# Optimization experiments

Measured on AMD Instinct MI355X. Metric: run time of the kernel, lower is better.

Reference implementation:

```python
import jax, jax.numpy as jnp
import numpy as np

DIM = 32          # image/vq dim (ImageTransform3D default dim=32 == vq.layers[0].dim)
CODEBOOK = 1024   # number of codebook entries
TOTAL = 4194304   # flat weight-vector length (multiple of DIM)


def setup_inputs() -> dict:
    key = jax.random.key(0)
    k1, k2, k3 = jax.random.split(key, 3)
    weights = jax.random.normal(k1, (TOTAL,), dtype=jnp.float32)
    condition = jax.random.normal(k2, (1, DIM, TOTAL // DIM), dtype=jnp.float32)
    codebook = jax.random.normal(k3, (CODEBOOK, DIM), dtype=jnp.float32)
    return {"weights": weights, "condition": condition, "codebook": codebook}


def reference(weights, condition, codebook):
    # --- ImageTransform3D.forward: pad flat weights to a multiple of DIM, view (1, DIM, -1)
    pad = (-weights.shape[0]) % DIM  # static
    if pad:
        weights = jnp.concatenate([weights, jnp.zeros((pad,), weights.dtype)])
    img = weights.reshape(1, DIM, -1)
    # --- TokenTransform3D: subtract condition, flatten to tokens of size DIM
    x = (img - condition).reshape(-1, DIM)  # [N, DIM]
    # --- VectorQuantize (freeze_codebook, eval): nearest-neighbour lookup
    d = (
        jnp.sum(x * x, axis=-1, keepdims=True)
        - 2.0 * (x @ codebook.T)
        + jnp.sum(codebook * codebook, axis=-1)
    )
    indices = jnp.argmin(d, axis=-1)  # [N] int32
    return indices
```

## Files before the change

### kernel.cpp

```cpp
#include <hip/hip_runtime.h>

#define TOTAL     4194304
#define DIM       32
#define NTOK      (TOTAL / DIM)
#define NCODE     1024
#define CCODES    256
#define DELTA_EPS 2e-3f
#define FLAGBIT   0x40000000

typedef _Float16 half8   __attribute__((ext_vector_type(8)));
typedef float    floatx4 __attribute__((ext_vector_type(4)));

#define GLOAD_LDS16(g, l) \
    __builtin_amdgcn_global_load_lds((const __attribute__((address_space(1))) void*)(g), \
                                     (__attribute__((address_space(3))) void*)(l), 16, 0, 0)
#define GLOAD_LDS4(g, l) \
    __builtin_amdgcn_global_load_lds((const __attribute__((address_space(1))) void*)(g), \
                                     (__attribute__((address_space(3))) void*)(l), 4, 0, 0)

__global__ __launch_bounds__(64) void vq_prep(
    const float* __restrict__ cb, float* __restrict__ nhb,
    _Float16* __restrict__ Eh, _Float16* __restrict__ El,
    float* __restrict__ cbT)
{
    const int k = blockIdx.x * 64 + threadIdx.x;
    const float4* e4 = reinterpret_cast<const float4*>(cb) + (size_t)k * 8;
    float v[DIM];
    float4 t[8];
#pragma unroll
    for (int j = 0; j < 8; ++j) t[j] = e4[j];
#pragma unroll
    for (int j = 0; j < 8; ++j) {
        v[4 * j + 0] = t[j].x; v[4 * j + 1] = t[j].y;
        v[4 * j + 2] = t[j].z; v[4 * j + 3] = t[j].w;
    }
    float e2 = 0.0f;
#pragma unroll
    for (int i = 0; i < DIM; ++i) e2 = fmaf(v[i], v[i], e2);
    nhb[k] = -0.5f * e2;

#pragma unroll
    for (int j = 0; j < DIM; ++j) cbT[(size_t)j * NCODE + k] = v[j];

    const int chunk = k >> 8, within = k & 255;
    const int step = within >> 4, l15 = within & 15;
#pragma unroll
    for (int l4 = 0; l4 < 4; ++l4) {
        half8 h, lo;
#pragma unroll
        for (int j = 0; j < 8; ++j) {
            float x = v[l4 * 8 + j];
            _Float16 hh = (_Float16)x;
            h[j]  = hh;
            lo[j] = (_Float16)(x - (float)hh);
        }
        const int slot = chunk * 1024 + step * 64 + l4 * 16 + l15;
        *reinterpret_cast<half8*>(Eh + (size_t)slot * 8) = h;
        *reinterpret_cast<half8*>(El + (size_t)slot * 8) = lo;
    }
}

__global__ __launch_bounds__(256) __attribute__((amdgpu_num_vgpr(60))) void vq_main(
    const float* __restrict__ w, const float* __restrict__ c,
    const float* __restrict__ nhb, const _Float16* __restrict__ Eh,
    const _Float16* __restrict__ El, const float* __restrict__ cbT,
    int* __restrict__ out)
{
    __shared__ _Float16 sEh[1024 * 8];
    __shared__ _Float16 sEl[1024 * 8];
    __shared__ float    snh[CCODES];
    __shared__ int      sOut[128];
    __shared__ float    sXf[4][DIM];

    const int tid  = threadIdx.x;
    const int lane = tid & 63;
    const int wid  = tid >> 6;
    const int tok0 = blockIdx.x * 128;
    const int tokw = tok0 + wid * 32;
    const int l15  = lane & 15;
    const int l4   = lane >> 4;

    half8 xh[2], xl[2];
#pragma unroll
    for (int m = 0; m < 2; ++m) {
        const int token = tokw + m * 16 + l15;
        const float4* pw = reinterpret_cast<const float4*>(w + (size_t)token * DIM + l4 * 8);
        const float4* pc = reinterpret_cast<const float4*>(c + (size_t)token * DIM + l4 * 8);
        float4 a0 = pw[0], a1 = pw[1], b0 = pc[0], b1 = pc[1];
        float xs[8] = {a0.x - b0.x, a0.y - b0.y, a0.z - b0.z, a0.w - b0.w,
                       a1.x - b1.x, a1.y - b1.y, a1.z - b1.z, a1.w - b1.w};
#pragma unroll
        for (int j = 0; j < 8; ++j) {
            _Float16 h = (_Float16)xs[j];
            xh[m][j] = h;
            xl[m][j] = (_Float16)(xs[j] - (float)h);
        }
    }

    const float NEGINF = __uint_as_float(0xFF800000u);
    float best[8], second[8];
#pragma unroll
    for (int q = 0; q < 8; ++q) { best[q] = NEGINF; second[q] = NEGINF; }

    for (int ch = 0; ch < 4; ++ch) {
        if (ch) __syncthreads();
        {
            const _Float16* gh = Eh + (size_t)ch * 8192;
            const _Float16* gl = El + (size_t)ch * 8192;
#pragma unroll
            for (int r2 = 0; r2 < 4; ++r2) {
                const int slot = r2 * 256 + wid * 64;
                GLOAD_LDS16(gh + (size_t)(slot + lane) * 8, sEh + (size_t)slot * 8);
                GLOAD_LDS16(gl + (size_t)(slot + lane) * 8, sEl + (size_t)slot * 8);
            }
            GLOAD_LDS4(nhb + ch * CCODES + wid * 64 + lane, snh + wid * 64);
        }
        __syncthreads();

#pragma unroll
        for (int sp = 0; sp < 8; ++sp) {
            const int sA = 2 * sp, sB = 2 * sp + 1;
            const half8 ehA = *reinterpret_cast<const half8*>(sEh + (size_t)(sA * 64 + lane) * 8);
            const half8 elA = *reinterpret_cast<const half8*>(sEl + (size_t)(sA * 64 + lane) * 8);
            const half8 ehB = *reinterpret_cast<const half8*>(sEh + (size_t)(sB * 64 + lane) * 8);
            const half8 elB = *reinterpret_cast<const half8*>(sEl + (size_t)(sB * 64 + lane) * 8);
            const float nhA = snh[sA * 16 + l15];
            const float nhB = snh[sB * 16 + l15];
            const unsigned ixA = 1023u - (unsigned)(ch * CCODES + sA * 16 + l15);
            const unsigned ixB = ixA - 16u;
            const floatx4 nA = {nhA, nhA, nhA, nhA};
            const floatx4 nB = {nhB, nhB, nhB, nhB};
#pragma unroll
            for (int m = 0; m < 2; ++m) {
                floatx4 aA = __builtin_amdgcn_mfma_f32_16x16x32_f16(xh[m], ehA, nA, 0, 0, 0);
                aA = __builtin_amdgcn_mfma_f32_16x16x32_f16(xl[m], ehA, aA, 0, 0, 0);
                aA = __builtin_amdgcn_mfma_f32_16x16x32_f16(xh[m], elA, aA, 0, 0, 0);
                floatx4 aB = __builtin_amdgcn_mfma_f32_16x16x32_f16(xh[m], ehB, nB, 0, 0, 0);
                aB = __builtin_amdgcn_mfma_f32_16x16x32_f16(xl[m], ehB, aB, 0, 0, 0);
                aB = __builtin_amdgcn_mfma_f32_16x16x32_f16(xh[m], elB, aB, 0, 0, 0);
#pragma unroll
                for (int r = 0; r < 4; ++r) {
                    const int q = m * 4 + r;
                    float pA = __uint_as_float((__float_as_uint(aA[r]) & 0xFFFFFC00u) | ixA);
                    float pB = __uint_as_float((__float_as_uint(aB[r]) & 0xFFFFFC00u) | ixB);
                    second[q] = fmaxf(second[q], __builtin_amdgcn_fmed3f(pA, pB, best[q]));
                    best[q]   = fmaxf(fmaxf(best[q], pA), pB);
                }
            }
        }
    }

#pragma unroll
    for (int sh = 1; sh < 16; sh <<= 1) {
#pragma unroll
        for (int q = 0; q < 8; ++q) {
            float bB = __shfl_xor(best[q], sh);
            float sB = __shfl_xor(second[q], sh);
            second[q] = fmaxf(fmaxf(second[q], sB), fminf(best[q], bB));
            best[q]   = fmaxf(best[q], bB);
        }
    }

    if (l15 == 0) {
#pragma unroll
        for (int m = 0; m < 2; ++m) {
#pragma unroll
            for (int r = 0; r < 4; ++r) {
                const int q = m * 4 + r;
                unsigned ub = __float_as_uint(best[q]);
                unsigned us = __float_as_uint(second[q]);
                float bv = __uint_as_float(ub & 0xFFFFFC00u);
                float sv = __uint_as_float(us & 0xFFFFFC00u);
                int eb = (int)((ub >> 23) & 255u);
                int es = (int)((us >> 23) & 255u);
                int em = eb > es ? eb : es;
                em = em > 12 ? em : 12;
                float thr = __uint_as_float((unsigned)(em - 12) << 23) + DELTA_EPS;
                int k = 1023 - (int)(ub & 1023u);
                sOut[wid * 32 + m * 16 + l4 * 4 + r] = ((bv - sv) < thr) ? (k | FLAGBIT) : k;
            }
        }
    }
    __syncthreads();

    int v0 = sOut[lane];
    int v1 = sOut[64 + lane];
    unsigned long long f0 = __ballot((v0 & FLAGBIT) != 0);
    unsigned long long f1 = __ballot((v1 & FLAGBIT) != 0);
    if (!(v0 & FLAGBIT)) out[tok0 + lane]      = v0;
    if (!(v1 & FLAGBIT)) out[tok0 + 64 + lane] = v1;

    int j = 0;
#pragma unroll
    for (int h = 0; h < 2; ++h) {
        unsigned long long m = h ? f1 : f0;
        while (m) {
            const int pos = __ffsll(m) - 1;
            m &= m - 1;
            if ((j++ & 3) != wid) continue;
            const int token = tok0 + h * 64 + pos;

            if (lane < DIM)
                sXf[wid][lane] = w[(size_t)token * DIM + lane] - c[(size_t)token * DIM + lane];

            float x2 = 0.f;
#pragma unroll
            for (int i = 0; i < DIM; ++i) x2 = fmaf(sXf[wid][i], sXf[wid][i], x2);

            float dmin = INFINITY;
            int   kbest = 0;
            for (int i = 0; i < 16; ++i) {
                const int k = lane + 64 * i;
                float dot = 0.f;
#pragma unroll
                for (int jj = 0; jj < DIM; ++jj)
                    dot = fmaf(sXf[wid][jj], cbT[(size_t)jj * NCODE + k], dot);
                float e2 = -2.0f * nhb[k];
                float dd = fmaf(-2.0f, dot, x2) + e2;
                if (dd < dmin) { dmin = dd; kbest = k; }
            }
#pragma unroll
            for (int sh = 1; sh < 64; sh <<= 1) {
                float dB = __shfl_xor(dmin, sh);
                int   iB = __shfl_xor(kbest, sh);
                bool take = (dB < dmin) || (dB == dmin && iB < kbest);
                dmin = take ? dB : dmin;
                kbest = take ? iB : kbest;
            }
            if (lane == 0) out[token] = kbest;
        }
    }
}

extern "C" void kernel_launch(void* const* d_in, const int* in_sizes, int n_in,
                              void* d_out, int out_size, void* d_ws, size_t ws_size,
                              hipStream_t stream) {
    const float* w  = (const float*)d_in[0];
    const float* c  = (const float*)d_in[1];
    const float* cb = (const float*)d_in[2];
    int* out = (int*)d_out;

    char* wsb = (char*)d_ws;
    float*    nhb = (float*)wsb;
    _Float16* Eh  = (_Float16*)(wsb + 4096);
    _Float16* El  = (_Float16*)(wsb + 4096 + 65536);
    float*    cbT = (float*)(wsb + 4096 + 65536 + 65536);

    vq_prep<<<NCODE / 64, 64, 0, stream>>>(cb, nhb, Eh, El, cbT);
    vq_main<<<NTOK / 128, 256, 0, stream>>>(w, c, nhb, Eh, El, cbT, out);
}
```

Measured before the change: 50.84 us.

## Split codebook across two wave groups per block with 512 threads

Doubles the block to 512 threads: two groups of four waves each handle the same 128 tokens but scan half of the codebook (512 codes) each, in 128-code chunks staged into per-group LDS buffers. Per-token best/second candidates from both halves are merged through shared memory before the flagging and fallback path. This halves the serial MFMA/argmax work per wave and adds waves per CU to hide latency. The cost is that every token's x values are loaded twice, plus an extra merge step and barrier.

```diff
diff --git a/kernel.cpp b/kernel.cpp
--- a/kernel.cpp
+++ b/kernel.cpp
@@ -4,7 +4,7 @@
 #define DIM       32
 #define NTOK      (TOTAL / DIM)
 #define NCODE     1024
-#define CCODES    256
+#define CCODES    128
 #define DELTA_EPS 2e-3f
 #define FLAGBIT   0x40000000
 
@@ -42,7 +42,7 @@
 #pragma unroll
     for (int j = 0; j < DIM; ++j) cbT[(size_t)j * NCODE + k] = v[j];
 
-    const int chunk = k >> 8, within = k & 255;
+    const int chunk = k >> 7, within = k & 127;
     const int step = within >> 4, l15 = within & 15;
 #pragma unroll
     for (int l4 = 0; l4 < 4; ++l4) {
@@ -54,29 +54,32 @@
             h[j]  = hh;
             lo[j] = (_Float16)(x - (float)hh);
         }
-        const int slot = chunk * 1024 + step * 64 + l4 * 16 + l15;
+        const int slot = chunk * 512 + step * 64 + l4 * 16 + l15;
         *reinterpret_cast<half8*>(Eh + (size_t)slot * 8) = h;
         *reinterpret_cast<half8*>(El + (size_t)slot * 8) = lo;
     }
 }
 
-__global__ __launch_bounds__(256) __attribute__((amdgpu_num_vgpr(60))) void vq_main(
+__global__ __launch_bounds__(512) __attribute__((amdgpu_num_vgpr(60))) void vq_main(
     const float* __restrict__ w, const float* __restrict__ c,
     const float* __restrict__ nhb, const _Float16* __restrict__ Eh,
     const _Float16* __restrict__ El, const float* __restrict__ cbT,
     int* __restrict__ out)
 {
-    __shared__ _Float16 sEh[1024 * 8];
-    __shared__ _Float16 sEl[1024 * 8];
-    __shared__ float    snh[CCODES];
+    __shared__ _Float16 sEh[2][512 * 8];
+    __shared__ _Float16 sEl[2][512 * 8];
+    __shared__ float    snh[2][CCODES];
+    __shared__ float2   sBS[2][128];
     __shared__ int      sOut[128];
-    __shared__ float    sXf[4][DIM];
+    __shared__ float    sXf[8][DIM];
 
     const int tid  = threadIdx.x;
     const int lane = tid & 63;
     const int wid  = tid >> 6;
+    const int grp  = wid >> 2;
+    const int wg   = wid & 3;
     const int tok0 = blockIdx.x * 128;
-    const int tokw = tok0 + wid * 32;
+    const int tokw = tok0 + wg * 32;
     const int l15  = lane & 15;
     const int l4   = lane >> 4;
 
@@ -102,30 +105,34 @@
 #pragma unroll
     for (int q = 0; q < 8; ++q) { best[q] = NEGINF; second[q] = NEGINF; }
 
-    for (int ch = 0; ch < 4; ++ch) {
-        if (ch) __syncthreads();
+    _Float16* myEh = &sEh[grp][0];
+    _Float16* myEl = &sEl[grp][0];
+
+    for (int cc = 0; cc < 4; ++cc) {
+        const int ch = grp * 4 + cc;
+        if (cc) __syncthreads();
         {
-            const _Float16* gh = Eh + (size_t)ch * 8192;
-            const _Float16* gl = El + (size_t)ch * 8192;
-#pragma unroll
-            for (int r2 = 0; r2 < 4; ++r2) {
-                const int slot = r2 * 256 + wid * 64;
-                GLOAD_LDS16(gh + (size_t)(slot + lane) * 8, sEh + (size_t)slot * 8);
-                GLOAD_LDS16(gl + (size_t)(slot + lane) * 8, sEl + (size_t)slot * 8);
-            }
-            GLOAD_LDS4(nhb + ch * CCODES + wid * 64 + lane, snh + wid * 64);
+            const _Float16* gh = Eh + (size_t)ch * 4096;
+            const _Float16* gl = El + (size_t)ch * 4096;
+#pragma unroll
+            for (int r2 = 0; r2 < 2; ++r2) {
+                const int slot = r2 * 256 + wg * 64;
+                GLOAD_LDS16(gh + (size_t)(slot + lane) * 8, myEh + (size_t)slot * 8);
+                GLOAD_LDS16(gl + (size_t)(slot + lane) * 8, myEl + (size_t)slot * 8);
+            }
+            if (wg < 2) GLOAD_LDS4(nhb + ch * CCODES + wg * 64 + lane, &snh[grp][wg * 64]);
         }
         __syncthreads();
 
 #pragma unroll
-        for (int sp = 0; sp < 8; ++sp) {
+        for (int sp = 0; sp < 4; ++sp) {
             const int sA = 2 * sp, sB = 2 * sp + 1;
-            const half8 ehA = *reinterpret_cast<const half8*>(sEh + (size_t)(sA * 64 + lane) * 8);
-            const half8 elA = *reinterpret_cast<const half8*>(sEl + (size_t)(sA * 64 + lane) * 8);
-            const half8 ehB = *reinterpret_cast<const half8*>(sEh + (size_t)(sB * 64 + lane) * 8);
-            const half8 elB = *reinterpret_cast<const half8*>(sEl + (size_t)(sB * 64 + lane) * 8);
-            const float nhA = snh[sA * 16 + l15];
-            const float nhB = snh[sB * 16 + l15];
+            const half8 ehA = *reinterpret_cast<const half8*>(myEh + (size_t)(sA * 64 + lane) * 8);
+            const half8 elA = *reinterpret_cast<const half8*>(myEl + (size_t)(sA * 64 + lane) * 8);
+            const half8 ehB = *reinterpret_cast<const half8*>(myEh + (size_t)(sB * 64 + lane) * 8);
+            const half8 elB = *reinterpret_cast<const half8*>(myEl + (size_t)(sB * 64 + lane) * 8);
+            const float nhA = snh[grp][sA * 16 + l15];
+            const float nhB = snh[grp][sB * 16 + l15];
             const unsigned ixA = 1023u - (unsigned)(ch * CCODES + sA * 16 + l15);
             const unsigned ixB = ixA - 16u;
             const floatx4 nA = {nhA, nhA, nhA, nhA};
@@ -167,19 +174,28 @@
 #pragma unroll
             for (int r = 0; r < 4; ++r) {
                 const int q = m * 4 + r;
-                unsigned ub = __float_as_uint(best[q]);
-                unsigned us = __float_as_uint(second[q]);
-                float bv = __uint_as_float(ub & 0xFFFFFC00u);
-                float sv = __uint_as_float(us & 0xFFFFFC00u);
-                int eb = (int)((ub >> 23) & 255u);
-                int es = (int)((us >> 23) & 255u);
-                int em = eb > es ? eb : es;
-                em = em > 12 ? em : 12;
-                float thr = __uint_as_float((unsigned)(em - 12) << 23) + DELTA_EPS;
-                int k = 1023 - (int)(ub & 1023u);
-                sOut[wid * 32 + m * 16 + l4 * 4 + r] = ((bv - sv) < thr) ? (k | FLAGBIT) : k;
-            }
-        }
+                sBS[grp][wg * 32 + m * 16 + l4 * 4 + r] = make_float2(best[q], second[q]);
+            }
+        }
+    }
+    __syncthreads();
+
+    if (tid < 128) {
+        float2 A = sBS[0][tid];
+        float2 B = sBS[1][tid];
+        float bst = fmaxf(A.x, B.x);
+        float snd = fmaxf(fmaxf(A.y, B.y), fminf(A.x, B.x));
+        unsigned ub = __float_as_uint(bst);
+        unsigned us = __float_as_uint(snd);
+        float bv = __uint_as_float(ub & 0xFFFFFC00u);
+        float sv = __uint_as_float(us & 0xFFFFFC00u);
+        int eb = (int)((ub >> 23) & 255u);
+        int es = (int)((us >> 23) & 255u);
+        int em = eb > es ? eb : es;
+        em = em > 12 ? em : 12;
+        float thr = __uint_as_float((unsigned)(em - 12) << 23) + DELTA_EPS;
+        int k = 1023 - (int)(ub & 1023u);
+        sOut[tid] = ((bv - sv) < thr) ? (k | FLAGBIT) : k;
     }
     __syncthreads();
 
@@ -187,8 +203,8 @@
     int v1 = sOut[64 + lane];
     unsigned long long f0 = __ballot((v0 & FLAGBIT) != 0);
     unsigned long long f1 = __ballot((v1 & FLAGBIT) != 0);
-    if (!(v0 & FLAGBIT)) out[tok0 + lane]      = v0;
-    if (!(v1 & FLAGBIT)) out[tok0 + 64 + lane] = v1;
+    if (wid == 0 && !(v0 & FLAGBIT)) out[tok0 + lane]      = v0;
+    if (wid == 1 && !(v1 & FLAGBIT)) out[tok0 + 64 + lane] = v1;
 
     int j = 0;
 #pragma unroll
@@ -197,7 +213,7 @@
         while (m) {
             const int pos = __ffsll(m) - 1;
             m &= m - 1;
-            if ((j++ & 3) != wid) continue;
+            if ((j++ & 7) != wid) continue;
             const int token = tok0 + h * 64 + pos;
 
             if (lane < DIM)
@@ -210,14 +226,14 @@
             float dmin = INFINITY;
             int   kbest = 0;
             for (int i = 0; i < 16; ++i) {
-                const int k = lane + 64 * i;
+                const int kk = lane + 64 * i;
                 float dot = 0.f;
 #pragma unroll
                 for (int jj = 0; jj < DIM; ++jj)
-                    dot = fmaf(sXf[wid][jj], cbT[(size_t)jj * NCODE + k], dot);
-                float e2 = -2.0f * nhb[k];
+                    dot = fmaf(sXf[wid][jj], cbT[(size_t)jj * NCODE + kk], dot);
+                float e2 = -2.0f * nhb[kk];
                 float dd = fmaf(-2.0f, dot, x2) + e2;
-                if (dd < dmin) { dmin = dd; kbest = k; }
+                if (dd < dmin) { dmin = dd; kbest = kk; }
             }
 #pragma unroll
             for (int sh = 1; sh < 64; sh <<= 1) {
@@ -244,8 +260,8 @@
     float*    nhb = (float*)wsb;
     _Float16* Eh  = (_Float16*)(wsb + 4096);
     _Float16* El  = (_Float16*)(wsb + 4096 + 65536);
-    float*    cbT = (float*)(wsb + 4096 + 65536 + 65536);
+    float*    cbT = (float*)(wsb + 4096 + 2 * 65536);
 
     vq_prep<<<NCODE / 64, 64, 0, stream>>>(cb, nhb, Eh, El, cbT);
-    vq_main<<<NTOK / 128, 256, 0, stream>>>(w, c, nhb, Eh, El, cbT, out);
+    vq_main<<<NTOK / 128, 512, 0, stream>>>(w, c, nhb, Eh, El, cbT, out);
 }
```

New measurement: 58.77 us. 15.6% more time.

## Double-buffer codebook chunks in LDS to overlap loads with MFMA compute

Applied to the files above, without the earlier changes.

Halves the codebook chunk size to 128 codes and splits the LDS codebook buffers into two halves. The loads for the next chunk are issued before the MFMA distance pass runs on the current chunk, which is meant to hide global-to-LDS load latency behind compute. The prep kernel's slot layout is changed to match the new chunk size. In exchange there are twice as many chunks, each needing a block-wide barrier, and the chunk loop is fully unrolled, which grows code size under the tight VGPR cap.

```diff
diff --git a/kernel.cpp b/kernel.cpp
--- a/kernel.cpp
+++ b/kernel.cpp
@@ -4,7 +4,7 @@
 #define DIM       32
 #define NTOK      (TOTAL / DIM)
 #define NCODE     1024
-#define CCODES    256
+#define CCODES    128
 #define DELTA_EPS 2e-3f
 #define FLAGBIT   0x40000000
 
@@ -42,7 +42,7 @@
 #pragma unroll
     for (int j = 0; j < DIM; ++j) cbT[(size_t)j * NCODE + k] = v[j];
 
-    const int chunk = k >> 8, within = k & 255;
+    const int chunk = k >> 7, within = k & 127;
     const int step = within >> 4, l15 = within & 15;
 #pragma unroll
     for (int l4 = 0; l4 < 4; ++l4) {
@@ -54,7 +54,7 @@
             h[j]  = hh;
             lo[j] = (_Float16)(x - (float)hh);
         }
-        const int slot = chunk * 1024 + step * 64 + l4 * 16 + l15;
+        const int slot = chunk * 512 + step * 64 + l4 * 16 + l15;
         *reinterpret_cast<half8*>(Eh + (size_t)slot * 8) = h;
         *reinterpret_cast<half8*>(El + (size_t)slot * 8) = lo;
     }
@@ -66,9 +66,9 @@
     const _Float16* __restrict__ El, const float* __restrict__ cbT,
     int* __restrict__ out)
 {
-    __shared__ _Float16 sEh[1024 * 8];
-    __shared__ _Float16 sEl[1024 * 8];
-    __shared__ float    snh[CCODES];
+    __shared__ _Float16 sEh[2][512 * 8];
+    __shared__ _Float16 sEl[2][512 * 8];
+    __shared__ float    snh[2][CCODES];
     __shared__ int      sOut[128];
     __shared__ float    sXf[4][DIM];
 
@@ -102,30 +102,37 @@
 #pragma unroll
     for (int q = 0; q < 8; ++q) { best[q] = NEGINF; second[q] = NEGINF; }
 
-    for (int ch = 0; ch < 4; ++ch) {
-        if (ch) __syncthreads();
-        {
-            const _Float16* gh = Eh + (size_t)ch * 8192;
-            const _Float16* gl = El + (size_t)ch * 8192;
-#pragma unroll
-            for (int r2 = 0; r2 < 4; ++r2) {
-                const int slot = r2 * 256 + wid * 64;
-                GLOAD_LDS16(gh + (size_t)(slot + lane) * 8, sEh + (size_t)slot * 8);
-                GLOAD_LDS16(gl + (size_t)(slot + lane) * 8, sEl + (size_t)slot * 8);
-            }
-            GLOAD_LDS4(nhb + ch * CCODES + wid * 64 + lane, snh + wid * 64);
-        }
-        __syncthreads();
-
-#pragma unroll
-        for (int sp = 0; sp < 8; ++sp) {
+#define STAGE(ch, b)                                                                     \
+    {                                                                                    \
+        const _Float16* gh = Eh + (size_t)(ch) * 4096;                                   \
+        const _Float16* gl = El + (size_t)(ch) * 4096;                                   \
+        _Pragma("unroll")                                                                \
+        for (int r2 = 0; r2 < 2; ++r2) {                                                 \
+            const int slot = r2 * 256 + wid * 64;                                        \
+            GLOAD_LDS16(gh + (size_t)(slot + lane) * 8, &sEh[b][(size_t)slot * 8]);      \
+            GLOAD_LDS16(gl + (size_t)(slot + lane) * 8, &sEl[b][(size_t)slot * 8]);      \
+        }                                                                                \
+        if (wid < 2) GLOAD_LDS4(nhb + (ch) * CCODES + wid * 64 + lane,                   \
+                                &snh[b][wid * 64]);                                      \
+    }
+
+    STAGE(0, 0);
+    __syncthreads();
+
+#pragma unroll
+    for (int ch = 0; ch < 8; ++ch) {
+        const int b = ch & 1;
+        if (ch < 7) STAGE(ch + 1, (ch + 1) & 1);
+
+#pragma unroll
+        for (int sp = 0; sp < 4; ++sp) {
             const int sA = 2 * sp, sB = 2 * sp + 1;
-            const half8 ehA = *reinterpret_cast<const half8*>(sEh + (size_t)(sA * 64 + lane) * 8);
-            const half8 elA = *reinterpret_cast<const half8*>(sEl + (size_t)(sA * 64 + lane) * 8);
-            const half8 ehB = *reinterpret_cast<const half8*>(sEh + (size_t)(sB * 64 + lane) * 8);
-            const half8 elB = *reinterpret_cast<const half8*>(sEl + (size_t)(sB * 64 + lane) * 8);
-            const float nhA = snh[sA * 16 + l15];
-            const float nhB = snh[sB * 16 + l15];
+            const half8 ehA = *reinterpret_cast<const half8*>(&sEh[b][(size_t)(sA * 64 + lane) * 8]);
+            const half8 elA = *reinterpret_cast<const half8*>(&sEl[b][(size_t)(sA * 64 + lane) * 8]);
+            const half8 ehB = *reinterpret_cast<const half8*>(&sEh[b][(size_t)(sB * 64 + lane) * 8]);
+            const half8 elB = *reinterpret_cast<const half8*>(&sEl[b][(size_t)(sB * 64 + lane) * 8]);
+            const float nhA = snh[b][sA * 16 + l15];
+            const float nhB = snh[b][sB * 16 + l15];
             const unsigned ixA = 1023u - (unsigned)(ch * CCODES + sA * 16 + l15);
             const unsigned ixB = ixA - 16u;
             const floatx4 nA = {nhA, nhA, nhA, nhA};
@@ -148,7 +155,9 @@
                 }
             }
         }
-    }
+        __syncthreads();
+    }
+#undef STAGE
 
 #pragma unroll
     for (int sh = 1; sh < 16; sh <<= 1) {
@@ -210,14 +219,14 @@
             float dmin = INFINITY;
             int   kbest = 0;
             for (int i = 0; i < 16; ++i) {
-                const int k = lane + 64 * i;
+                const int kk = lane + 64 * i;
                 float dot = 0.f;
 #pragma unroll
                 for (int jj = 0; jj < DIM; ++jj)
-                    dot = fmaf(sXf[wid][jj], cbT[(size_t)jj * NCODE + k], dot);
-                float e2 = -2.0f * nhb[k];
+                    dot = fmaf(sXf[wid][jj], cbT[(size_t)jj * NCODE + kk], dot);
+                float e2 = -2.0f * nhb[kk];
                 float dd = fmaf(-2.0f, dot, x2) + e2;
-                if (dd < dmin) { dmin = dd; kbest = k; }
+                if (dd < dmin) { dmin = dd; kbest = kk; }
             }
 #pragma unroll
             for (int sh = 1; sh < 64; sh <<= 1) {
@@ -244,7 +253,7 @@
     float*    nhb = (float*)wsb;
     _Float16* Eh  = (_Float16*)(wsb + 4096);
     _Float16* El  = (_Float16*)(wsb + 4096 + 65536);
-    float*    cbT = (float*)(wsb + 4096 + 65536 + 65536);
+    float*    cbT = (float*)(wsb + 4096 + 2 * 65536);
 
     vq_prep<<<NCODE / 64, 64, 0, stream>>>(cb, nhb, Eh, El, cbT);
     vq_main<<<NTOK / 128, 256, 0, stream>>>(w, c, nhb, Eh, El, cbT, out);
```

Result: slower. 51.91 us (+2.1%).
